# Performance work log

Measured on AMD Instinct MI355X. Metric: run time of the kernel, lower is better.

Reference implementation:

```python
import jax, jax.numpy as jnp
import numpy as np

N_NODES = 50000
N_EDGES = 800000
N_GRAPHS = 2048
IN_DIM = 128
HID = 256
N_LAYERS = 4
BN_EPS = 1e-5


def setup_inputs() -> dict:
    key = jax.random.key(0)
    ks = jax.random.split(key, 12)
    x = jax.random.normal(ks[0], (N_NODES, IN_DIM), dtype=jnp.float32)
    edge_index = jax.random.randint(ks[1], (2, N_EDGES), 0, N_NODES, dtype=jnp.int64)
    batch = jnp.sort(jax.random.randint(ks[2], (N_NODES,), 0, N_GRAPHS, dtype=jnp.int64))
    convW0 = jax.random.normal(ks[3], (IN_DIM, HID), dtype=jnp.float32) * (IN_DIM ** -0.5)
    convWs = jax.random.normal(ks[4], (N_LAYERS - 1, HID, HID), dtype=jnp.float32) * (HID ** -0.5)
    convB = jnp.zeros((N_LAYERS, HID), dtype=jnp.float32)
    bn_gamma = jnp.ones((N_LAYERS, HID), dtype=jnp.float32)
    bn_beta = jnp.zeros((N_LAYERS, HID), dtype=jnp.float32)
    bn_mean = jnp.zeros((N_LAYERS, HID), dtype=jnp.float32)
    bn_var = jax.random.uniform(ks[5], (N_LAYERS, HID), dtype=jnp.float32, minval=0.5, maxval=1.5)
    lin1W = jax.random.normal(ks[6], (HID, HID // 2), dtype=jnp.float32) * (HID ** -0.5)
    lin1b = jnp.zeros((HID // 2,), dtype=jnp.float32)
    lin2W = jax.random.normal(ks[7], (HID // 2, 1), dtype=jnp.float32) * ((HID // 2) ** -0.5)
    lin2b = jnp.zeros((1,), dtype=jnp.float32)
    return dict(x=x, edge_index=edge_index, batch=batch, convW0=convW0, convWs=convWs,
                convB=convB, bn_gamma=bn_gamma, bn_beta=bn_beta, bn_mean=bn_mean,
                bn_var=bn_var, lin1W=lin1W, lin1b=lin1b, lin2W=lin2W, lin2b=lin2b)


def reference(x, edge_index, batch, convW0, convWs, convB, bn_gamma, bn_beta,
              bn_mean, bn_var, lin1W, lin1b, lin2W, lin2b):
    N = x.shape[0]
    src, dst = edge_index[0], edge_index[1]
    # degree with self-loops (PyG GCNConv default add_self_loops=True)
    deg = jnp.zeros((N,), dtype=x.dtype).at[dst].add(1.0) + 1.0
    dinv = deg ** -0.5
    enorm = (dinv[src] * dinv[dst])[:, None]      # [E,1]
    self_norm = (1.0 / deg)[:, None]              # [N,1] self-loop weight

    def gcn_conv(h, W, b):
        h = h @ W                                 # [N,H]
        agg = jax.ops.segment_sum(h[src] * enorm, dst, num_segments=N)
        return agg + h * self_norm + b

    Ws = [convW0] + [convWs[i] for i in range(convWs.shape[0])]
    for l in range(N_LAYERS):
        x = gcn_conv(x, Ws[l], convB[l])
        # eval-mode BatchNorm1d
        x = (x - bn_mean[l]) * jax.lax.rsqrt(bn_var[l] + BN_EPS) * bn_gamma[l] + bn_beta[l]
        x = jax.nn.relu(x)
        # dropout: identity in eval mode

    # global_mean_pool over graph ids
    sums = jax.ops.segment_sum(x, batch, num_segments=N_GRAPHS)      # [G,H]
    cnts = jax.ops.segment_sum(jnp.ones((N,), x.dtype), batch, num_segments=N_GRAPHS)
    pooled = sums / jnp.maximum(cnts, 1.0)[:, None]

    h = jax.nn.relu(pooled @ lin1W + lin1b)
    out = (h @ lin2W + lin2b).squeeze(-1)          # [G]
    return out
```

## Files before the change

### kernel.cpp

```cpp
#include <hip/hip_runtime.h>

#define N_NODES 50000
#define N_EDGES 800000
#define N_GRAPHS 2048
#define IN_DIM 128
#define HID 256
#define N_LAYERS 4
#define BN_EPS 1e-5f
#define NBIN 128
#define WSCALE 64.0f

#define EDGE_BLKS 3125
#define NODE_BLKS 196

typedef unsigned short ushort_t;
typedef float f32x4 __attribute__((ext_vector_type(4)));
typedef unsigned int u32x4 __attribute__((ext_vector_type(4)));
typedef _Float16 f16x8 __attribute__((ext_vector_type(8)));
typedef _Float16 f16x4 __attribute__((ext_vector_type(4)));

__device__ __forceinline__ void gl_lds16(const ushort_t* g, ushort_t* l) {
    __builtin_amdgcn_global_load_lds(
        (const __attribute__((address_space(1))) void*)g,
        (__attribute__((address_space(3))) void*)l, 16, 0, 0);
}

__global__ __launch_bounds__(256) void k_degboundsprep(const int* __restrict__ dst,
                                                       int* __restrict__ degi,
                                                       const int* __restrict__ batch,
                                                       int* __restrict__ gstart,
                                                       int* __restrict__ gend,
                                                       const float* __restrict__ gamma,
                                                       const float* __restrict__ beta,
                                                       const float* __restrict__ mean,
                                                       const float* __restrict__ var,
                                                       const float* __restrict__ bias,
                                                       const float* __restrict__ W0,
                                                       const float* __restrict__ Ws,
                                                       const float* __restrict__ x,
                                                       float* __restrict__ scale,
                                                       float* __restrict__ shift,
                                                       _Float16* __restrict__ Wh,
                                                       _Float16* __restrict__ X16) {
    int bid = blockIdx.x;
    if (bid < EDGE_BLKS) {
        int e = bid * 256 + threadIdx.x;
        if (e < N_EDGES) atomicAdd(&degi[dst[e]], 1);
        return;
    }
    if (bid < EDGE_BLKS + NODE_BLKS) {
        int n = (bid - EDGE_BLKS) * 256 + threadIdx.x;
        if (n >= N_NODES) return;
        int g = batch[n];
        if (n == 0 || batch[n - 1] != g) gstart[g] = n;
        if (n == N_NODES - 1 || batch[n + 1] != g) gend[g] = n + 1;
        return;
    }
    int id = (bid - EDGE_BLKS - NODE_BLKS) * 256 + threadIdx.x;
    if (id < N_LAYERS * HID) {
        float s = gamma[id] * rsqrtf(var[id] + BN_EPS);
        scale[id] = s / WSCALE;
        shift[id] = beta[id] + (bias[id] - mean[id]) * s;
        return;
    }
    id -= N_LAYERS * HID;
    const int WT = 128 * 256 + 3 * 256 * 256;
    if (id < WT) {
        float v;
        if (id < 32768) {
            int n = id >> 7, k = id & 127;
            v = W0[k * 256 + n];
        } else {
            int t = id - 32768;
            int l = t >> 16;
            int r = t & 65535;
            int n = r >> 8, k = r & 255;
            v = Ws[l * 65536 + k * 256 + n];
        }
        Wh[id] = (_Float16)(v * WSCALE);
        return;
    }
    id -= WT;
    const int total4 = N_NODES * IN_DIM / 4;
    if (id < total4) {
        float4 v = ((const float4*)x)[id];
        int n = id >> 5;
        int c0 = (id & 31) * 4;
        f16x4 o;
        o.x = (_Float16)v.x; o.y = (_Float16)v.y; o.z = (_Float16)v.z; o.w = (_Float16)v.w;
        *(f16x4*)(X16 + (size_t)(c0 >> 5) * (N_NODES * 32) + (size_t)n * 32 + (c0 & 31)) = o;
    }
}

__global__ __launch_bounds__(256) void k_nodeprep(const int* __restrict__ degi,
                                                  float* __restrict__ dinv,
                                                  float* __restrict__ selfn,
                                                  int* __restrict__ bins, int N) {
    __shared__ int lbin[NBIN];
    int t = threadIdx.x;
    if (t < NBIN) lbin[t] = 0;
    __syncthreads();
    int n = blockIdx.x * 256 + t;
    if (n < N) {
        int dg = degi[n];
        float d = 1.0f + (float)dg;
        dinv[n] = 1.0f / sqrtf(d);
        selfn[n] = 1.0f / d;
        atomicAdd(&lbin[min(dg, NBIN - 1)], 1);
    }
    __syncthreads();
    if (t < NBIN && lbin[t] > 0) atomicAdd(&bins[t], lbin[t]);
}

__global__ void k_binscan(const int* __restrict__ bins, int* __restrict__ binstart,
                          int* __restrict__ bincur, int* __restrict__ edgebase) {
    int t = threadIdx.x & 63;
    int d0 = 2 * t, d1 = 2 * t + 1;
    int a = bins[d0], b = bins[d1];
    int ea = a * d0, eb = b * d1;
    int s = a + b, es = ea + eb;
    int ps = s, pe = es;
    #pragma unroll
    for (int off = 1; off < 64; off <<= 1) {
        int u = __shfl_up(ps, off, 64);
        int v = __shfl_up(pe, off, 64);
        if (t >= off) { ps += u; pe += v; }
    }
    int exs = ps - s, exe = pe - es;
    binstart[d0] = exs;     bincur[d0] = exs;     edgebase[d0] = exe;
    binstart[d1] = exs + a; bincur[d1] = exs + a; edgebase[d1] = exe + ea;
}

__global__ __launch_bounds__(256) void k_assign(const int* __restrict__ degi,
                                                const int* __restrict__ binstart,
                                                const int* __restrict__ edgebase,
                                                const int* __restrict__ bins,
                                                int* __restrict__ bincur,
                                                const float* __restrict__ dinv,
                                                int* __restrict__ perm,
                                                int4* __restrict__ invmeta,
                                                int2* __restrict__ meta, int* __restrict__ cursor,
                                                int N) {
    __shared__ int lbin[NBIN];
    __shared__ int lbase[NBIN];
    int t = threadIdx.x;
    if (t < NBIN) lbin[t] = 0;
    __syncthreads();
    int n = blockIdx.x * 256 + t;
    int d = 0, lrank = 0;
    if (n < N) {
        d = min(degi[n], NBIN - 1);
        lrank = atomicAdd(&lbin[d], 1);
    }
    __syncthreads();
    if (t < NBIN && lbin[t] > 0) lbase[t] = atomicAdd(&bincur[t], lbin[t]);
    __syncthreads();
    if (n < N) {
        int slot = lbase[d] + lrank;
        int base = edgebase[d] + (slot - binstart[d]);
        perm[slot] = n;
        int2 m;
        m.x = base;
        m.y = bins[d] | (d << 20);
        meta[slot] = m;
        int4 im;
        im.x = base;
        im.y = bins[d];
        im.z = __float_as_int(dinv[n]);
        im.w = 0;
        invmeta[n] = im;
        cursor[n] = 0;
    }
}

__global__ __launch_bounds__(256) void k_fill(const int* __restrict__ src,
                                              const int* __restrict__ dst,
                                              const float* __restrict__ dinv,
                                              const int4* __restrict__ invmeta,
                                              int* __restrict__ cursor,
                                              unsigned int* __restrict__ edata) {
    int e = blockIdx.x * 256 + threadIdx.x;
    if (e >= N_EDGES) return;
    int s = src[e], d = dst[e];
    int4 im = invmeta[d];
    int j = atomicAdd(&cursor[d], 1);
    float wdd = __int_as_float(im.z);
    float wss = dinv[s];
    int pos = im.x + j * im.y;
    _Float16 hw = (_Float16)(wss * wdd);
    edata[pos] = ((unsigned int)__builtin_bit_cast(unsigned short, hw) << 16) |
                 (unsigned int)s;
}

__global__ __launch_bounds__(256) void k_gemm(const _Float16* __restrict__ A,
                                              const _Float16* __restrict__ Wh,
                                              const float* __restrict__ bnscale,
                                              const float* __restrict__ bnshift,
                                              _Float16* __restrict__ X16, int K) {
    __shared__ _Float16 sm[2 * 128 * 64];
    _Float16* tA  = sm;
    _Float16* tWh = sm + 8192;

    int tid = threadIdx.x;
    int lane = tid & 63;
    int w = tid >> 6;
    int wrow = w & 1, wcol = w >> 1;
    int row0 = blockIdx.x * 128;
    int col0 = blockIdx.y * 128;

    int srow8 = lane >> 3;
    int sch8 = lane & 7;

    f32x4 acc[4][4] = {};
    int m = lane & 15, q = lane >> 4;

    for (int k0 = 0; k0 < K; k0 += 64) {
        #pragma unroll
        for (int ii = 0; ii < 8; ++ii) {
            int G = w * 8 + ii;
            int mat = G >> 4;
            int grp = G & 15;
            const _Float16* gs = (mat == 0) ? A : Wh;
            _Float16* ld = sm + mat * 8192;
            int rb = (mat == 0) ? row0 : col0;
            int rl = (mat == 0) ? N_NODES : (col0 + 128);
            int r = grp * 8 + srow8;
            int grow = rb + r;
            int gch = sch8 ^ (r & 7);
            if (grow < rl)
                gl_lds16((const ushort_t*)(gs + (size_t)grow * K + k0 + gch * 8),
                         (ushort_t*)(ld + grp * 512));
        }
        __syncthreads();

        #pragma unroll
        for (int t = 0; t < 2; ++t) {
            f16x8 af[4], whf[4];
            #pragma unroll
            for (int r = 0; r < 4; ++r) {
                int rr = wrow * 64 + r * 16 + m;
                int c = t * 4 + q;
                af[r] = *(const f16x8*)(tA + rr * 64 + ((c ^ (rr & 7)) << 3));
            }
            #pragma unroll
            for (int fc = 0; fc < 4; ++fc) {
                int nn = wcol * 64 + fc * 16 + m;
                int c = t * 4 + q;
                whf[fc] = *(const f16x8*)(tWh + nn * 64 + ((c ^ (nn & 7)) << 3));
            }
            #pragma unroll
            for (int r = 0; r < 4; ++r)
                #pragma unroll
                for (int fc = 0; fc < 4; ++fc)
                    acc[r][fc] = __builtin_amdgcn_mfma_f32_16x16x32_f16(af[r], whf[fc], acc[r][fc], 0, 0, 0);
        }
        __syncthreads();
    }

    #pragma unroll
    for (int r = 0; r < 4; ++r) {
        int mrow = row0 + wrow * 64 + r * 16 + (lane >> 4) * 4;
        #pragma unroll
        for (int c = 0; c < 4; ++c) {
            int n = col0 + wcol * 64 + c * 16 + (lane & 15);
            float sc = bnscale[n];
            float sh = bnshift[n];
            f32x4 v = acc[r][c];
            _Float16* base = X16 + (size_t)(n >> 5) * (N_NODES * 32) + (n & 31);
            #pragma unroll
            for (int g = 0; g < 4; ++g)
                if (mrow + g < N_NODES)
                    base[(size_t)(mrow + g) * 32] =
                        (_Float16)fmaxf(fmaf(v[g], sc, sh), 0.f);
        }
    }
}

#define GNB 782

__global__ __launch_bounds__(256) void k_gather(const _Float16* __restrict__ Xc,
                                                const int2* __restrict__ meta,
                                                const unsigned int* __restrict__ edata,
                                                const int* __restrict__ perm,
                                                const float* __restrict__ selfn,
                                                _Float16* __restrict__ A,
                                                int K, int cshift) {
    int bid = blockIdx.x;
    int chunk = bid & ((1 << cshift) - 1);
    int nb = (GNB - 1) - (bid >> cshift);
    const _Float16* Hc = Xc + (size_t)chunk * (N_NODES * 32);
    int slot = nb * 64 + (threadIdx.x >> 2);
    if (slot >= N_NODES) return;
    int node = perm[slot];
    int2 m = meta[slot];
    int q8 = (threadIdx.x & 3) * 8;

    int stride = m.y & 0xFFFFF;
    int deg = m.y >> 20;
    const unsigned int* ep = edata + m.x;
    float sn = selfn[node];

    float acc[8];
    {
        f16x8 hv = *(const f16x8*)(Hc + (size_t)node * 32 + q8);
        #pragma unroll
        for (int i = 0; i < 8; ++i) acc[i] = (float)hv[i] * sn;
    }

    int j = 0;
    for (; j + 7 < deg; j += 8) {
        unsigned int e[8];
        #pragma unroll
        for (int i = 0; i < 8; ++i)
            e[i] = ep[(size_t)(j + i) * stride];
        f16x8 a[8];
        #pragma unroll
        for (int i = 0; i < 8; ++i)
            a[i] = *(const f16x8*)(Hc + (size_t)(e[i] & 0xFFFFu) * 32 + q8);
        #pragma unroll
        for (int i = 0; i < 8; ++i) {
            float w = (float)__builtin_bit_cast(_Float16, (unsigned short)(e[i] >> 16));
            #pragma unroll
            for (int c = 0; c < 8; ++c) acc[c] = fmaf((float)a[i][c], w, acc[c]);
        }
    }
    if (j + 3 < deg) {
        unsigned int e[4];
        #pragma unroll
        for (int i = 0; i < 4; ++i)
            e[i] = ep[(size_t)(j + i) * stride];
        f16x8 a[4];
        #pragma unroll
        for (int i = 0; i < 4; ++i)
            a[i] = *(const f16x8*)(Hc + (size_t)(e[i] & 0xFFFFu) * 32 + q8);
        #pragma unroll
        for (int i = 0; i < 4; ++i) {
            float w = (float)__builtin_bit_cast(_Float16, (unsigned short)(e[i] >> 16));
            #pragma unroll
            for (int c = 0; c < 8; ++c) acc[c] = fmaf((float)a[i][c], w, acc[c]);
        }
        j += 4;
    }
    for (; j < deg; ++j) {
        unsigned int e0 = ep[(size_t)j * stride];
        f16x8 a0 = *(const f16x8*)(Hc + (size_t)(e0 & 0xFFFFu) * 32 + q8);
        float w0 = (float)__builtin_bit_cast(_Float16, (unsigned short)(e0 >> 16));
        #pragma unroll
        for (int i = 0; i < 8; ++i) acc[i] = fmaf((float)a0[i], w0, acc[i]);
    }

    f16x8 o;
    #pragma unroll
    for (int i = 0; i < 8; ++i) o[i] = (_Float16)acc[i];
    u32x4 uv = *(u32x4*)&o;
    __builtin_nontemporal_store(uv, (u32x4*)(A + (size_t)node * K + chunk * 32 + q8));
}

__global__ __launch_bounds__(128) void k_poolmlp(const _Float16* __restrict__ X16,
                                                 const int* __restrict__ gstart,
                                                 const int* __restrict__ gend,
                                                 const float* __restrict__ W1,
                                                 const float* __restrict__ b1,
                                                 const float* __restrict__ W2,
                                                 const float* __restrict__ b2,
                                                 float* __restrict__ out) {
    __shared__ float prow[HID];
    __shared__ float hred[2];
    int g = blockIdx.x;
    int s = gstart[g], e = gend[g];
    int j = threadIdx.x;
    const _Float16* p0 = X16 + (size_t)(j >> 5) * (N_NODES * 32) + (j & 31);
    const _Float16* p1 = X16 + (size_t)((j >> 5) + 4) * (N_NODES * 32) + (j & 31);
    float a0 = 0.f, a1 = 0.f;
    for (int n = s; n < e; ++n) {
        a0 += (float)p0[(size_t)n * 32];
        a1 += (float)p1[(size_t)n * 32];
    }
    float inv = 1.0f / fmaxf((float)(e - s), 1.0f);
    prow[j] = a0 * inv;
    prow[j + 128] = a1 * inv;
    __syncthreads();
    float acc = 0.f;
    #pragma unroll 8
    for (int k = 0; k < HID; ++k) acc += prow[k] * W1[k * 128 + j];
    float h = fmaxf(acc + b1[j], 0.f);
    float p = h * W2[j];
    #pragma unroll
    for (int off = 32; off > 0; off >>= 1) p += __shfl_down(p, off, 64);
    if ((j & 63) == 0) hred[j >> 6] = p;
    __syncthreads();
    if (j == 0) out[g] = hred[0] + hred[1] + b2[0];
}

extern "C" void kernel_launch(void* const* d_in, const int* in_sizes, int n_in,
                              void* d_out, int out_size, void* d_ws, size_t ws_size,
                              hipStream_t stream) {
    const float* x      = (const float*)d_in[0];
    const int*   ei     = (const int*)d_in[1];
    const int*   batch  = (const int*)d_in[2];
    const float* convW0 = (const float*)d_in[3];
    const float* convWs = (const float*)d_in[4];
    const float* convB  = (const float*)d_in[5];
    const float* gamma  = (const float*)d_in[6];
    const float* beta   = (const float*)d_in[7];
    const float* mean   = (const float*)d_in[8];
    const float* var    = (const float*)d_in[9];
    const float* lin1W  = (const float*)d_in[10];
    const float* lin1b  = (const float*)d_in[11];
    const float* lin2W  = (const float*)d_in[12];
    const float* lin2b  = (const float*)d_in[13];
    float* out = (float*)d_out;

    const int* src = ei;
    const int* dst = ei + N_EDGES;

    const int WTOT = 128 * 256 + 3 * 256 * 256;

    char* wsb = (char*)d_ws;
    _Float16* x16a = (_Float16*)wsb;
    _Float16* x16b = x16a + (size_t)N_NODES * HID;
    _Float16* Ab   = x16b + (size_t)N_NODES * HID;
    _Float16* Wh16 = Ab + (size_t)N_NODES * HID;
    _Float16* Wl16 = Wh16 + WTOT;
    float* dinv    = (float*)(Wl16 + WTOT);
    float* selfn   = dinv + N_NODES;
    float* bnscale = selfn + N_NODES;
    float* bnshift = bnscale + N_LAYERS * HID;
    int*   degi    = (int*)(bnshift + N_LAYERS * HID);
    int*   bins    = degi + N_NODES;
    int*   gstart  = bins + NBIN;
    int*   gend    = gstart + N_GRAPHS;
    int*   binstart= gend + N_GRAPHS;
    int*   bincur  = binstart + NBIN;
    int*   edgebase= bincur + NBIN;
    int*   cursor  = edgebase + NBIN;
    int*   perm    = cursor + N_NODES;
    int2*  meta    = (int2*)(perm + N_NODES);
    int4*  invmeta = (int4*)(meta + N_NODES);
    unsigned int* edata = (unsigned int*)(invmeta + N_NODES);

    hipMemsetAsync(degi, 0, (size_t)(N_NODES + NBIN + 2 * N_GRAPHS) * 4, stream);

    const int PREP_TOT = N_LAYERS * HID + WTOT + N_NODES * IN_DIM / 4;
    const int PREP_BLKS = (PREP_TOT + 255) / 256;
    k_degboundsprep<<<EDGE_BLKS + NODE_BLKS + PREP_BLKS, 256, 0, stream>>>(
        dst, degi, batch, gstart, gend,
        gamma, beta, mean, var, convB, convW0, convWs, x,
        bnscale, bnshift, Wh16, x16a);
    k_nodeprep<<<NODE_BLKS, 256, 0, stream>>>(degi, dinv, selfn, bins, N_NODES);
    k_binscan<<<1, 64, 0, stream>>>(bins, binstart, bincur, edgebase);
    k_assign<<<NODE_BLKS, 256, 0, stream>>>(degi, binstart, edgebase, bins, bincur, dinv,
                                            perm, invmeta, meta, cursor, N_NODES);

    k_fill<<<EDGE_BLKS, 256, 0, stream>>>(src, dst, dinv, invmeta, cursor, edata);

    dim3 gg((N_NODES + 127) / 128, 2);
    _Float16* cur = x16a;
    for (int l = 0; l < N_LAYERS; ++l) {
        int K = (l == 0) ? IN_DIM : HID;
        int nchunk = K / 32;
        int cshift = (l == 0) ? 2 : 3;
        size_t woff = (l == 0) ? 0 : (size_t)(32768 + (l - 1) * 65536);
        k_gather<<<nchunk * GNB, 256, 0, stream>>>(cur, meta, edata, perm, selfn,
                                                   Ab, K, cshift);
        _Float16* nxt = (cur == x16a) ? x16b : x16a;
        k_gemm<<<gg, 256, 0, stream>>>(Ab, Wh16 + woff,
                                       bnscale + l * HID, bnshift + l * HID, nxt, K);
        cur = nxt;
    }

    k_poolmlp<<<N_GRAPHS, 128, 0, stream>>>(cur, gstart, gend, lin1W, lin1b, lin2W, lin2b, out);
}
```

Measured before the change: 448.2 us.

## Reuse degree atomics as edge ranks, drop LDS staging in GEMM, unroll pooling

The degree-count atomic now records each edge's rank within its destination, so the fill kernel reads that rank instead of doing a second atomic on a cursor array. The GEMM drops its LDS-staged, swizzled tiles and loads MFMA operands directly from global memory in 32-wide K steps. The pooling loop is unrolled by four with separate accumulators. The GEMM change gives up LDS reuse and synchronisation in favour of uncoalesced strided global loads, and it also drops the row bound check on A for the last partial tile.

```diff
diff --git a/kernel.cpp b/kernel.cpp
--- a/kernel.cpp
+++ b/kernel.cpp
@@ -19,14 +19,9 @@
 typedef _Float16 f16x8 __attribute__((ext_vector_type(8)));
 typedef _Float16 f16x4 __attribute__((ext_vector_type(4)));
 
-__device__ __forceinline__ void gl_lds16(const ushort_t* g, ushort_t* l) {
-    __builtin_amdgcn_global_load_lds(
-        (const __attribute__((address_space(1))) void*)g,
-        (__attribute__((address_space(3))) void*)l, 16, 0, 0);
-}
-
 __global__ __launch_bounds__(256) void k_degboundsprep(const int* __restrict__ dst,
                                                        int* __restrict__ degi,
+                                                       int* __restrict__ erank,
                                                        const int* __restrict__ batch,
                                                        int* __restrict__ gstart,
                                                        int* __restrict__ gend,
@@ -45,7 +40,7 @@
     int bid = blockIdx.x;
     if (bid < EDGE_BLKS) {
         int e = bid * 256 + threadIdx.x;
-        if (e < N_EDGES) atomicAdd(&degi[dst[e]], 1);
+        if (e < N_EDGES) erank[e] = atomicAdd(&degi[dst[e]], 1);
         return;
     }
     if (bid < EDGE_BLKS + NODE_BLKS) {
@@ -139,7 +134,7 @@
                                                 const float* __restrict__ dinv,
                                                 int* __restrict__ perm,
                                                 int4* __restrict__ invmeta,
-                                                int2* __restrict__ meta, int* __restrict__ cursor,
+                                                int2* __restrict__ meta,
                                                 int N) {
     __shared__ int lbin[NBIN];
     __shared__ int lbase[NBIN];
@@ -169,7 +164,6 @@
         im.z = __float_as_int(dinv[n]);
         im.w = 0;
         invmeta[n] = im;
-        cursor[n] = 0;
     }
 }
 
@@ -177,13 +171,13 @@
                                               const int* __restrict__ dst,
                                               const float* __restrict__ dinv,
                                               const int4* __restrict__ invmeta,
-                                              int* __restrict__ cursor,
+                                              const int* __restrict__ erank,
                                               unsigned int* __restrict__ edata) {
     int e = blockIdx.x * 256 + threadIdx.x;
     if (e >= N_EDGES) return;
     int s = src[e], d = dst[e];
     int4 im = invmeta[d];
-    int j = atomicAdd(&cursor[d], 1);
+    int j = erank[e];
     float wdd = __int_as_float(im.z);
     float wss = dinv[s];
     int pos = im.x + j * im.y;
@@ -197,64 +191,32 @@
                                               const float* __restrict__ bnscale,
                                               const float* __restrict__ bnshift,
                                               _Float16* __restrict__ X16, int K) {
-    __shared__ _Float16 sm[2 * 128 * 64];
-    _Float16* tA  = sm;
-    _Float16* tWh = sm + 8192;
-
     int tid = threadIdx.x;
     int lane = tid & 63;
     int w = tid >> 6;
     int wrow = w & 1, wcol = w >> 1;
     int row0 = blockIdx.x * 128;
     int col0 = blockIdx.y * 128;
-
-    int srow8 = lane >> 3;
-    int sch8 = lane & 7;
+    int m = lane & 15, q = lane >> 4;
 
     f32x4 acc[4][4] = {};
-    int m = lane & 15, q = lane >> 4;
-
-    for (int k0 = 0; k0 < K; k0 += 64) {
-        #pragma unroll
-        for (int ii = 0; ii < 8; ++ii) {
-            int G = w * 8 + ii;
-            int mat = G >> 4;
-            int grp = G & 15;
-            const _Float16* gs = (mat == 0) ? A : Wh;
-            _Float16* ld = sm + mat * 8192;
-            int rb = (mat == 0) ? row0 : col0;
-            int rl = (mat == 0) ? N_NODES : (col0 + 128);
-            int r = grp * 8 + srow8;
-            int grow = rb + r;
-            int gch = sch8 ^ (r & 7);
-            if (grow < rl)
-                gl_lds16((const ushort_t*)(gs + (size_t)grow * K + k0 + gch * 8),
-                         (ushort_t*)(ld + grp * 512));
-        }
-        __syncthreads();
-
-        #pragma unroll
-        for (int t = 0; t < 2; ++t) {
-            f16x8 af[4], whf[4];
+
+    const _Float16* Abase = A + (size_t)(row0 + wrow * 64 + m) * K + q * 8;
+    const _Float16* Wbase = Wh + (size_t)(col0 + wcol * 64 + m) * K + q * 8;
+
+    for (int k0 = 0; k0 < K; k0 += 32) {
+        f16x8 af[4], whf[4];
+        #pragma unroll
+        for (int r = 0; r < 4; ++r)
+            af[r] = *(const f16x8*)(Abase + (size_t)(r * 16) * K + k0);
+        #pragma unroll
+        for (int c = 0; c < 4; ++c)
+            whf[c] = *(const f16x8*)(Wbase + (size_t)(c * 16) * K + k0);
+        #pragma unroll
+        for (int r = 0; r < 4; ++r)
             #pragma unroll
-            for (int r = 0; r < 4; ++r) {
-                int rr = wrow * 64 + r * 16 + m;
-                int c = t * 4 + q;
-                af[r] = *(const f16x8*)(tA + rr * 64 + ((c ^ (rr & 7)) << 3));
-            }
-            #pragma unroll
-            for (int fc = 0; fc < 4; ++fc) {
-                int nn = wcol * 64 + fc * 16 + m;
-                int c = t * 4 + q;
-                whf[fc] = *(const f16x8*)(tWh + nn * 64 + ((c ^ (nn & 7)) << 3));
-            }
-            #pragma unroll
-            for (int r = 0; r < 4; ++r)
-                #pragma unroll
-                for (int fc = 0; fc < 4; ++fc)
-                    acc[r][fc] = __builtin_amdgcn_mfma_f32_16x16x32_f16(af[r], whf[fc], acc[r][fc], 0, 0, 0);
-        }
-        __syncthreads();
+            for (int c = 0; c < 4; ++c)
+                acc[r][c] = __builtin_amdgcn_mfma_f32_16x16x32_f16(af[r], whf[c], acc[r][c], 0, 0, 0);
     }
 
     #pragma unroll
@@ -371,11 +333,24 @@
     int j = threadIdx.x;
     const _Float16* p0 = X16 + (size_t)(j >> 5) * (N_NODES * 32) + (j & 31);
     const _Float16* p1 = X16 + (size_t)((j >> 5) + 4) * (N_NODES * 32) + (j & 31);
-    float a0 = 0.f, a1 = 0.f;
-    for (int n = s; n < e; ++n) {
+    float a0 = 0.f, a1 = 0.f, b0 = 0.f, b1v = 0.f, c0 = 0.f, c1 = 0.f, d0 = 0.f, d1 = 0.f;
+    int n = s;
+    for (; n + 3 < e; n += 4) {
         a0 += (float)p0[(size_t)n * 32];
         a1 += (float)p1[(size_t)n * 32];
-    }
+        b0 += (float)p0[(size_t)(n + 1) * 32];
+        b1v += (float)p1[(size_t)(n + 1) * 32];
+        c0 += (float)p0[(size_t)(n + 2) * 32];
+        c1 += (float)p1[(size_t)(n + 2) * 32];
+        d0 += (float)p0[(size_t)(n + 3) * 32];
+        d1 += (float)p1[(size_t)(n + 3) * 32];
+    }
+    for (; n < e; ++n) {
+        a0 += (float)p0[(size_t)n * 32];
+        a1 += (float)p1[(size_t)n * 32];
+    }
+    a0 = (a0 + b0) + (c0 + d0);
+    a1 = (a1 + b1v) + (c1 + d1);
     float inv = 1.0f / fmaxf((float)(e - s), 1.0f);
     prow[j] = a0 * inv;
     prow[j + 128] = a1 * inv;
@@ -433,26 +408,26 @@
     int*   binstart= gend + N_GRAPHS;
     int*   bincur  = binstart + NBIN;
     int*   edgebase= bincur + NBIN;
-    int*   cursor  = edgebase + NBIN;
-    int*   perm    = cursor + N_NODES;
+    int*   perm    = edgebase + NBIN;
     int2*  meta    = (int2*)(perm + N_NODES);
     int4*  invmeta = (int4*)(meta + N_NODES);
-    unsigned int* edata = (unsigned int*)(invmeta + N_NODES);
+    int*   erank   = (int*)(invmeta + N_NODES);
+    unsigned int* edata = (unsigned int*)(erank + N_EDGES);
 
     hipMemsetAsync(degi, 0, (size_t)(N_NODES + NBIN + 2 * N_GRAPHS) * 4, stream);
 
     const int PREP_TOT = N_LAYERS * HID + WTOT + N_NODES * IN_DIM / 4;
     const int PREP_BLKS = (PREP_TOT + 255) / 256;
     k_degboundsprep<<<EDGE_BLKS + NODE_BLKS + PREP_BLKS, 256, 0, stream>>>(
-        dst, degi, batch, gstart, gend,
+        dst, degi, erank, batch, gstart, gend,
         gamma, beta, mean, var, convB, convW0, convWs, x,
         bnscale, bnshift, Wh16, x16a);
     k_nodeprep<<<NODE_BLKS, 256, 0, stream>>>(degi, dinv, selfn, bins, N_NODES);
     k_binscan<<<1, 64, 0, stream>>>(bins, binstart, bincur, edgebase);
     k_assign<<<NODE_BLKS, 256, 0, stream>>>(degi, binstart, edgebase, bins, bincur, dinv,
-                                            perm, invmeta, meta, cursor, N_NODES);
-
-    k_fill<<<EDGE_BLKS, 256, 0, stream>>>(src, dst, dinv, invmeta, cursor, edata);
+                                            perm, invmeta, meta, N_NODES);
+
+    k_fill<<<EDGE_BLKS, 256, 0, stream>>>(src, dst, dinv, invmeta, erank, edata);
 
     dim3 gg((N_NODES + 127) / 128, 2);
     _Float16* cur = x16a;
```

Measured after the change: 464.5 us. 3.6% more time.
